# Optimization experiments

Hardware: AMD Instinct MI355X
Metric: run time of the kernel (lower is better)

## Reference

```python
import jax, jax.numpy as jnp
import numpy as np

B, C = 4194304, 6
DEMI = C // 2            # demi_len = preds.shape[1] / 2
THRESH = 0.65            # confidence threshold from the original loop
PENALTY_WEIGHT = 0.1


def setup_inputs() -> dict:
    key = jax.random.key(0)
    k1, k2 = jax.random.split(key)
    preds = jax.random.normal(k1, (B, C), dtype=jnp.float32)
    labels = jax.random.randint(k2, (B,), 0, C)
    targets = jax.nn.one_hot(labels, C, dtype=jnp.float32)  # CE with probability targets
    return {"preds": preds, "targets": targets}


def reference(preds, targets):
    # base_loss: torch.nn.CrossEntropyLoss with probability targets, mean reduction
    logp = jax.nn.log_softmax(preds, axis=-1)
    base_loss = -jnp.mean(jnp.sum(targets * logp, axis=-1))

    # --- vectorized replica of the per-row Python loop ---
    s = jax.nn.sigmoid(preds)
    sR, sL = s[:, :DEMI], s[:, DEMI:]
    maxR = jnp.max(sR, axis=1)
    idxR = jnp.argmax(sR, axis=1)
    maxL = jnp.max(sL, axis=1)
    idxL = jnp.argmax(sL, axis=1)

    r_set = maxR > THRESH
    l_set = maxL > THRESH
    none_set = (~r_set) & (~l_set)
    r_wins = maxR > maxL  # strict >, else-branch picks left (matches original)

    useR = (r_set | (none_set & r_wins)).astype(jnp.float32)
    useL = (l_set | (none_set & ~r_wins)).astype(jnp.float32)

    pvR = jax.nn.one_hot(idxR, DEMI, dtype=jnp.float32) * useR[:, None]
    pvL = jax.nn.one_hot(idxL, DEMI, dtype=jnp.float32) * useL[:, None]
    # if both halves exceed threshold, row sums to 2 -> divided by its sum (0.5 each)
    both = r_set & l_set
    scale = jnp.where(both, 0.5, 1.0)[:, None]
    pv = jnp.concatenate([pvR, pvL], axis=1) * scale  # [B, 6]

    # penalty: original uses hardcoded :3 / 3: splits and whole-batch target sums
    t_left = jnp.sum(targets[:, :3]) > 0
    t_right = jnp.sum(targets[:, 3:]) > 0
    left_fn = (jnp.sum(pv[:, :3], axis=1) == 0) & t_left
    # right check reads prediction_vector[:, 3:].sum() at iteration j, i.e. rows 0..j
    right_cum = jnp.cumsum(jnp.sum(pv[:, 3:], axis=1))
    right_fn = (right_cum == 0) & t_right
    penalty_fn = jnp.sum((left_fn | right_fn).astype(jnp.float32))

    # penalty is a Python float in the original -> constant w.r.t. autodiff
    penalty = PENALTY_WEIGHT * penalty_fn
    return base_loss + jax.lax.stop_gradient(penalty)
```

## Files before the change

### kernel.cpp

```cpp
#include <hip/hip_runtime.h>
#include <cstdint>
#include <climits>

static constexpr float kLogitThresh = 0.61903920840622351f;
static constexpr int NB = 2048;

__device__ __forceinline__ void row_op(
    const float p[6], const float t[6], int row,
    float& lossSum, int& cnt, int& minK, int& tl, int& tr) {
  float mR = fmaxf(fmaxf(p[0], p[1]), p[2]);
  float mL = fmaxf(fmaxf(p[3], p[4]), p[5]);
  bool rs = mR > kLogitThresh;
  bool ls = mL > kLogitThresh;
  bool none = (!rs) && (!ls);
  bool rwins = mR > mL;
  bool useR = rs || (none && rwins);
  bool useL = ls || (none && !rwins);
  if (!useR) cnt++;
  if (useL && row < minK) minK = row;
  float tsumL = t[0] + t[1] + t[2];
  float tsumR = t[3] + t[4] + t[5];
  if (tsumL > 0.0f) tl = 1;
  if (tsumR > 0.0f) tr = 1;
  float m = fmaxf(mR, mL);
  float se = 0.0f, tp = 0.0f, ts = 0.0f;
#pragma unroll
  for (int j = 0; j < 6; ++j) {
    se += __expf(p[j] - m);
    tp += t[j] * p[j];
    ts += t[j];
  }
  float lse = m + __logf(se);
  lossSum += lse * ts - tp;
}

__global__ __launch_bounds__(256) void loss_main(
    const float* __restrict__ preds, const float* __restrict__ targets,
    int npairs,
    float* __restrict__ pLoss, int* __restrict__ pCnt,
    int* __restrict__ pMinK, int* __restrict__ pTl, int* __restrict__ pTr) {
  int tid = blockIdx.x * blockDim.x + threadIdx.x;
  int stride = gridDim.x * blockDim.x;
  float lossSum = 0.0f;
  int cnt = 0;
  int minK = INT_MAX;
  int tl = 0, tr = 0;

  for (int q = tid; q < npairs; q += stride) {
    size_t base = (size_t)q * 12;
    float4 a  = *reinterpret_cast<const float4*>(preds + base);
    float4 b  = *reinterpret_cast<const float4*>(preds + base + 4);
    float4 c  = *reinterpret_cast<const float4*>(preds + base + 8);
    float4 ta = *reinterpret_cast<const float4*>(targets + base);
    float4 tb = *reinterpret_cast<const float4*>(targets + base + 4);
    float4 tc = *reinterpret_cast<const float4*>(targets + base + 8);
    {
      float p[6] = {a.x, a.y, a.z, a.w, b.x, b.y};
      float t[6] = {ta.x, ta.y, ta.z, ta.w, tb.x, tb.y};
      row_op(p, t, 2 * q, lossSum, cnt, minK, tl, tr);
    }
    {
      float p[6] = {b.z, b.w, c.x, c.y, c.z, c.w};
      float t[6] = {tb.z, tb.w, tc.x, tc.y, tc.z, tc.w};
      row_op(p, t, 2 * q + 1, lossSum, cnt, minK, tl, tr);
    }
  }

#pragma unroll
  for (int off = 32; off > 0; off >>= 1) {
    lossSum += __shfl_down(lossSum, off);
    cnt     += __shfl_down(cnt, off);
    minK    = min(minK, __shfl_down(minK, off));
    tl      |= __shfl_down(tl, off);
    tr      |= __shfl_down(tr, off);
  }

  __shared__ float wLoss[4];
  __shared__ int wCnt[4], wMinK[4], wTl[4], wTr[4];
  int wave = threadIdx.x >> 6;
  int lane = threadIdx.x & 63;
  if (lane == 0) {
    wLoss[wave] = lossSum; wCnt[wave] = cnt; wMinK[wave] = minK;
    wTl[wave] = tl; wTr[wave] = tr;
  }
  __syncthreads();
  if (threadIdx.x == 0) {
    pLoss[blockIdx.x] = wLoss[0] + wLoss[1] + wLoss[2] + wLoss[3];
    pCnt[blockIdx.x]  = wCnt[0] + wCnt[1] + wCnt[2] + wCnt[3];
    pMinK[blockIdx.x] = min(min(wMinK[0], wMinK[1]), min(wMinK[2], wMinK[3]));
    pTl[blockIdx.x]   = wTl[0] | wTl[1] | wTl[2] | wTl[3];
    pTr[blockIdx.x]   = wTr[0] | wTr[1] | wTr[2] | wTr[3];
  }
}

__global__ __launch_bounds__(256) void reduce_final(
    const float* __restrict__ pLoss, const int* __restrict__ pCnt,
    const int* __restrict__ pMinK, const int* __restrict__ pTl,
    const int* __restrict__ pTr, float* __restrict__ out, int B) {
  double L = 0.0;
  int cnt = 0, mk = INT_MAX, tl = 0, tr = 0;
  for (int i = threadIdx.x; i < NB; i += 256) {
    L   += (double)pLoss[i];
    cnt += pCnt[i];
    mk   = min(mk, pMinK[i]);
    tl  |= pTl[i];
    tr  |= pTr[i];
  }
#pragma unroll
  for (int off = 32; off > 0; off >>= 1) {
    L   += __shfl_down(L, off);
    cnt += __shfl_down(cnt, off);
    mk   = min(mk, __shfl_down(mk, off));
    tl  |= __shfl_down(tl, off);
    tr  |= __shfl_down(tr, off);
  }
  __shared__ double sL[4];
  __shared__ int sC[4], sM[4], sT[4], sR[4];
  int wave = threadIdx.x >> 6;
  int lane = threadIdx.x & 63;
  if (lane == 0) {
    sL[wave] = L; sC[wave] = cnt; sM[wave] = mk; sT[wave] = tl; sR[wave] = tr;
  }
  __syncthreads();
  if (threadIdx.x == 0) {
    double Lt = sL[0] + sL[1] + sL[2] + sL[3];
    int Cn = sC[0] + sC[1] + sC[2] + sC[3];
    int K  = min(min(sM[0], sM[1]), min(sM[2], sM[3]));
    int Tl = sT[0] | sT[1] | sT[2] | sT[3];
    int Tr = sR[0] | sR[1] | sR[2] | sR[3];
    if (K > B) K = B;
    double base = Lt / (double)B;
    double pen = 0.1 * ((Tl ? (double)Cn : 0.0) + (Tr ? (double)K : 0.0));
    out[0] = (float)(base + pen);
  }
}

extern "C" void kernel_launch(void* const* d_in, const int* in_sizes, int n_in,
                              void* d_out, int out_size, void* d_ws, size_t ws_size,
                              hipStream_t stream) {
  const float* preds   = (const float*)d_in[0];
  const float* targets = (const float*)d_in[1];
  float* out = (float*)d_out;

  float* pLoss = (float*)d_ws;
  int*   pCnt  = (int*)((char*)d_ws + NB * 4);
  int*   pMinK = (int*)((char*)d_ws + NB * 8);
  int*   pTl   = (int*)((char*)d_ws + NB * 12);
  int*   pTr   = (int*)((char*)d_ws + NB * 16);

  int B = in_sizes[0] / 6;
  int npairs = B / 2;

  hipLaunchKernelGGL(loss_main, dim3(NB), dim3(256), 0, stream,
                     preds, targets, npairs, pLoss, pCnt, pMinK, pTl, pTr);
  hipLaunchKernelGGL(reduce_final, dim3(1), dim3(256), 0, stream,
                     pLoss, pCnt, pMinK, pTl, pTr, out, B);
}
```

Before: 38.85 us.

## Stage row chunks through swizzled LDS for fully coalesced global loads

Each block now loads a 512-row chunk of preds and targets as contiguous float4s, one per lane with stride 256, writes them to LDS using an XOR-like swizzle, then reads back three consecutive float4s per thread to process two rows. The aim is to replace the old strided 48-byte-per-thread global access with fully coalesced loads, with the swizzle meant to avoid LDS bank conflicts. The grid also shrinks from 2048 to 1536 blocks. This adds two barriers per chunk and LDS traffic, and it assumes B is a multiple of 512.

```diff
diff --git a/kernel.cpp b/kernel.cpp
--- a/kernel.cpp
+++ b/kernel.cpp
@@ -1,9 +1,12 @@
 #include <hip/hip_runtime.h>
-#include <cstdint>
 #include <climits>
 
 static constexpr float kLogitThresh = 0.61903920840622351f;
-static constexpr int NB = 2048;
+static constexpr int NB = 1536;
+static constexpr int ROWS_PER_CHUNK = 512;
+static constexpr int F4_PER_CHUNK = 768;
+
+__device__ __forceinline__ int swz(int s) { return (s & ~7) | ((3 * s) & 7); }
 
 __device__ __forceinline__ void row_op(
     const float p[6], const float t[6], int row,
@@ -35,35 +38,51 @@
 }
 
 __global__ __launch_bounds__(256) void loss_main(
-    const float* __restrict__ preds, const float* __restrict__ targets,
-    int npairs,
+    const float4* __restrict__ gp, const float4* __restrict__ gt,
+    int nChunks,
     float* __restrict__ pLoss, int* __restrict__ pCnt,
     int* __restrict__ pMinK, int* __restrict__ pTl, int* __restrict__ pTr) {
-  int tid = blockIdx.x * blockDim.x + threadIdx.x;
-  int stride = gridDim.x * blockDim.x;
+  __shared__ float4 lp[F4_PER_CHUNK];
+  __shared__ float4 lt[F4_PER_CHUNK];
+  const int tid = threadIdx.x;
   float lossSum = 0.0f;
   int cnt = 0;
   int minK = INT_MAX;
   int tl = 0, tr = 0;
 
-  for (int q = tid; q < npairs; q += stride) {
-    size_t base = (size_t)q * 12;
-    float4 a  = *reinterpret_cast<const float4*>(preds + base);
-    float4 b  = *reinterpret_cast<const float4*>(preds + base + 4);
-    float4 c  = *reinterpret_cast<const float4*>(preds + base + 8);
-    float4 ta = *reinterpret_cast<const float4*>(targets + base);
-    float4 tb = *reinterpret_cast<const float4*>(targets + base + 4);
-    float4 tc = *reinterpret_cast<const float4*>(targets + base + 8);
+  for (int c = blockIdx.x; c < nChunks; c += gridDim.x) {
+    const int base = c * F4_PER_CHUNK;
+    float4 a0 = gp[base + tid];
+    float4 a1 = gp[base + tid + 256];
+    float4 a2 = gp[base + tid + 512];
+    float4 b0 = gt[base + tid];
+    float4 b1 = gt[base + tid + 256];
+    float4 b2 = gt[base + tid + 512];
+    lp[swz(tid)]       = a0;
+    lp[swz(tid + 256)] = a1;
+    lp[swz(tid + 512)] = a2;
+    lt[swz(tid)]       = b0;
+    lt[swz(tid + 256)] = b1;
+    lt[swz(tid + 512)] = b2;
+    __syncthreads();
+    float4 p0 = lp[swz(3 * tid)];
+    float4 p1 = lp[swz(3 * tid + 1)];
+    float4 p2 = lp[swz(3 * tid + 2)];
+    float4 t0 = lt[swz(3 * tid)];
+    float4 t1 = lt[swz(3 * tid + 1)];
+    float4 t2 = lt[swz(3 * tid + 2)];
+    int row0 = c * ROWS_PER_CHUNK + 2 * tid;
     {
-      float p[6] = {a.x, a.y, a.z, a.w, b.x, b.y};
-      float t[6] = {ta.x, ta.y, ta.z, ta.w, tb.x, tb.y};
-      row_op(p, t, 2 * q, lossSum, cnt, minK, tl, tr);
+      float p[6] = {p0.x, p0.y, p0.z, p0.w, p1.x, p1.y};
+      float t[6] = {t0.x, t0.y, t0.z, t0.w, t1.x, t1.y};
+      row_op(p, t, row0, lossSum, cnt, minK, tl, tr);
     }
     {
-      float p[6] = {b.z, b.w, c.x, c.y, c.z, c.w};
-      float t[6] = {tb.z, tb.w, tc.x, tc.y, tc.z, tc.w};
-      row_op(p, t, 2 * q + 1, lossSum, cnt, minK, tl, tr);
+      float p[6] = {p1.z, p1.w, p2.x, p2.y, p2.z, p2.w};
+      float t[6] = {t1.z, t1.w, t2.x, t2.y, t2.z, t2.w};
+      row_op(p, t, row0 + 1, lossSum, cnt, minK, tl, tr);
     }
+    __syncthreads();
   }
 
 #pragma unroll
@@ -138,8 +157,8 @@
 extern "C" void kernel_launch(void* const* d_in, const int* in_sizes, int n_in,
                               void* d_out, int out_size, void* d_ws, size_t ws_size,
                               hipStream_t stream) {
-  const float* preds   = (const float*)d_in[0];
-  const float* targets = (const float*)d_in[1];
+  const float4* preds   = (const float4*)d_in[0];
+  const float4* targets = (const float4*)d_in[1];
   float* out = (float*)d_out;
 
   float* pLoss = (float*)d_ws;
@@ -149,10 +168,10 @@
   int*   pTr   = (int*)((char*)d_ws + NB * 16);
 
   int B = in_sizes[0] / 6;
-  int npairs = B / 2;
+  int nChunks = B / ROWS_PER_CHUNK;
 
   hipLaunchKernelGGL(loss_main, dim3(NB), dim3(256), 0, stream,
-                     preds, targets, npairs, pLoss, pCnt, pMinK, pTl, pTr);
+                     preds, targets, nChunks, pLoss, pCnt, pMinK, pTl, pTr);
   hipLaunchKernelGGL(reduce_final, dim3(1), dim3(256), 0, stream,
                      pLoss, pCnt, pMinK, pTl, pTr, out, B);
 }
```

After: 39.09 us. No clear change (+0.6%).
